# Optimization experiments

Measured on AMD Instinct MI355X. Metric: run time of the kernel, lower is better.

The kernel has to match this reference:

```python
import jax, jax.numpy as jnp
import numpy as np

NUM_TYPES = 4
EPS = 1e-5
NEG_SLOPE = 0.01  # nn.LeakyReLU default


def hetero_linear(x, node_type, W, b):
    # x: [N, Cin], W: [T, Cin, Cout], b: [T, Cout]
    # Grouped GEMM via type-masked batched matmul (T is small and fixed).
    onehot = jax.nn.one_hot(node_type, NUM_TYPES, dtype=x.dtype)  # [N, T]
    xt = onehot.T[:, :, None] * x[None, :, :]                      # [T, N, Cin]
    y = jnp.einsum('tni,tio->no', xt, W)                           # [N, Cout]
    return y + b[node_type]


def hetero_batchnorm(x, node_type, gamma, beta):
    # Per-type batch statistics over the nodes of each type (training-mode BN).
    ones = jnp.ones((x.shape[0],), dtype=x.dtype)
    cnt = jax.ops.segment_sum(ones, node_type, num_segments=NUM_TYPES)      # [T]
    cnt = jnp.maximum(cnt, 1.0)
    s = jax.ops.segment_sum(x, node_type, num_segments=NUM_TYPES)           # [T, C]
    ss = jax.ops.segment_sum(x * x, node_type, num_segments=NUM_TYPES)      # [T, C]
    mean = s / cnt[:, None]
    var = ss / cnt[:, None] - mean * mean  # biased variance, as BN uses
    xn = (x - mean[node_type]) * jax.lax.rsqrt(var[node_type] + EPS)
    return xn * gamma[node_type] + beta[node_type]


def setup_inputs() -> dict:
    key = jax.random.key(0)
    ks = jax.random.split(key, 12)
    N, CIN, H, COUT, T = 32768, 256, 512, 256, NUM_TYPES
    x = jax.random.normal(ks[0], (N, CIN), dtype=jnp.float32)
    node_type = jax.random.randint(ks[1], (N,), 0, T, dtype=jnp.int32)
    def lin(k, ci, co):
        k1, k2 = jax.random.split(k)
        scale = 1.0 / np.sqrt(ci)
        W = jax.random.uniform(k1, (T, ci, co), jnp.float32, -scale, scale)
        b = jax.random.uniform(k2, (T, co), jnp.float32, -scale, scale)
        return W, b
    W1, b1 = lin(ks[2], CIN, H)
    W2, b2 = lin(ks[3], H, H)
    W3, b3 = lin(ks[4], H, COUT)
    gamma1 = jnp.ones((T, H), jnp.float32)
    beta1 = jnp.zeros((T, H), jnp.float32)
    gamma2 = jnp.ones((T, H), jnp.float32)
    beta2 = jnp.zeros((T, H), jnp.float32)
    return {"x": x, "node_type": node_type,
            "W1": W1, "b1": b1, "W2": W2, "b2": b2, "W3": W3, "b3": b3,
            "gamma1": gamma1, "beta1": beta1, "gamma2": gamma2, "beta2": beta2}


def reference(x, node_type, W1, b1, W2, b2, W3, b3, gamma1, beta1, gamma2, beta2):
    # Layer 1: HeteroLinear -> HeteroBatchNorm -> LeakyReLU (dropout p=0 -> identity)
    h = hetero_linear(x, node_type, W1, b1)
    h = hetero_batchnorm(h, node_type, gamma1, beta1)
    h = jax.nn.leaky_relu(h, NEG_SLOPE)
    # Layer 2
    h = hetero_linear(h, node_type, W2, b2)
    h = hetero_batchnorm(h, node_type, gamma2, beta2)
    h = jax.nn.leaky_relu(h, NEG_SLOPE)
    # Layer 3: plain_last -> no norm/act
    out = hetero_linear(h, node_type, W3, b3)
    return out
```

## Files before the change

kernel.cpp:

```cpp
#include <hip/hip_runtime.h>
#include <cstdint>
#include <cstddef>

#define N_NODES 32768
#define CIN 256
#define HDIM 512
#define COUT_F 256
#define NTYPE 4
#define ALIGN_SEG 256
#define NPAD (N_NODES + NTYPE * ALIGN_SEG)
#define NROWBLK (NPAD / 256)
#define BN_EPS 1e-5f
#define SLOPE 0.01f

typedef unsigned short u16;
typedef __attribute__((ext_vector_type(8))) short bf16x8;
typedef __attribute__((ext_vector_type(4))) float f32x4;
typedef __attribute__((ext_vector_type(4))) u16 u16x4;

#define GLOBAL_AS __attribute__((address_space(1)))
#define LDS_AS __attribute__((address_space(3)))
#define SBAR() __builtin_amdgcn_s_barrier()
#define SCHED() __builtin_amdgcn_sched_barrier(0)

__device__ __forceinline__ u16 f2bf(float f) {
  union { float f; unsigned u; } v{f};
  unsigned r = (v.u + 0x7FFF + ((v.u >> 16) & 1)) >> 16;
  return (u16)r;
}
__device__ __forceinline__ float bf2f(u16 b) {
  union { unsigned u; float f; } v;
  v.u = ((unsigned)b) << 16;
  return v.f;
}


__global__ void hist_kernel(const int* __restrict__ nt, int* __restrict__ blockHist) {
  __shared__ int h[NTYPE];
  int tid = threadIdx.x;
  if (tid < NTYPE) h[tid] = 0;
  __syncthreads();
  int i = blockIdx.x * 256 + tid;
  atomicAdd(&h[nt[i]], 1);
  __syncthreads();
  if (tid < NTYPE) blockHist[blockIdx.x * NTYPE + tid] = h[tid];
}

__global__ void scan_kernel(const int* __restrict__ blockHist, int* __restrict__ blockBase,
                            int* __restrict__ meta) {
  int tid = threadIdx.x;
  if (tid < NTYPE) {
    int run = 0;
    for (int b = 0; b < 128; ++b) {
      blockBase[b * NTYPE + tid] = run;
      run += blockHist[b * NTYPE + tid];
    }
    meta[tid] = run;
  }
  __syncthreads();
  if (tid == 0) {
    int s = 0;
    for (int t = 0; t < NTYPE; ++t) {
      meta[4 + t] = s;
      s += (meta[t] + ALIGN_SEG - 1) & ~(ALIGN_SEG - 1);
    }
    meta[8] = s;
  }
}

__global__ void rank_scatter_kernel(const int* __restrict__ nt, const int* __restrict__ blockBase,
                                    const int* __restrict__ meta, int* __restrict__ perm) {
  __shared__ int st[256];
  int tid = threadIdx.x;
  int i = blockIdx.x * 256 + tid;
  int t = nt[i];
  st[tid] = t;
  __syncthreads();
  int rank = 0;
  for (int j = 0; j < tid; ++j) rank += (st[j] == t) ? 1 : 0;
  perm[meta[4 + t] + blockBase[blockIdx.x * NTYPE + t] + rank] = i;
}

__global__ __launch_bounds__(256) void gather_kernel(const float* __restrict__ x,
                                                     const int* __restrict__ perm,
                                                     u16* __restrict__ xs) {
  int p = blockIdx.x * 4 + (threadIdx.x >> 6);
  int lane = threadIdx.x & 63;
  int src = perm[p];
  u16x4* dst = (u16x4*)(xs + (size_t)p * CIN);
  if (src < 0) {
    dst[lane] = (u16x4)0;
  } else {
    float4 v = ((const float4*)(x + (size_t)src * CIN))[lane];
    u16x4 o;
    o.x = f2bf(v.x); o.y = f2bf(v.y); o.z = f2bf(v.z); o.w = f2bf(v.w);
    dst[lane] = o;
  }
}

template <int K, int COUT>
__global__ __launch_bounds__(256) void wtrans_kernel(const float* __restrict__ W,
                                                     u16* __restrict__ Wt) {
  const int t = blockIdx.z;
  const int k0 = blockIdx.x * 32, c0 = blockIdx.y * 32;
  const float* __restrict__ Ws = W + (size_t)t * K * COUT;
  u16* __restrict__ Wd = Wt + (size_t)t * COUT * K;
  __shared__ float tile[32][33];
  int tid = threadIdx.x;
#pragma unroll
  for (int p = 0; p < 4; ++p) {
    int idx = p * 256 + tid;
    int r = idx >> 5, c = idx & 31;
    tile[r][c] = Ws[(size_t)(k0 + r) * COUT + c0 + c];
  }
  __syncthreads();
#pragma unroll
  for (int p = 0; p < 4; ++p) {
    int idx = p * 256 + tid;
    int r = idx >> 5, c = idx & 31;
    Wd[(size_t)(c0 + r) * K + k0 + c] = f2bf(tile[c][r]);
  }
}


template <int K, int COUT, int BN, bool SCATTER, bool STATS>
__global__ __launch_bounds__(512, 2) void mfma_gemm_kernel(
    const u16* __restrict__ A, const u16* __restrict__ Wt, const float* __restrict__ bias,
    u16* __restrict__ Yb, float* __restrict__ Yf, float* __restrict__ partS,
    float* __restrict__ partQ, const int* __restrict__ meta, const int* __restrict__ perm) {
  constexpr int JN = BN / 32;
  constexpr int PB = BN / 64;
  constexpr int GX = COUT / BN;
  constexpr int ASZ = 256 * 64;
  constexpr int BSZ = BN * 64;
  const int nwg = (int)(gridDim.x * gridDim.y);
  int l = (int)(blockIdx.y * gridDim.x + blockIdx.x);
  int lid = (l & 7) * (nwg >> 3) + (l >> 3);
  const int bx = lid % GX, by = lid / GX;
  const int col0 = bx * BN, row0 = by * 256;

  const int s1 = meta[5], s2 = meta[6], s3 = meta[7];
  const int t = row0 >= s3 ? 3 : (row0 >= s2 ? 2 : (row0 >= s1 ? 1 : 0));
  const int seg_end = meta[4 + t] + meta[t];
  const u16* __restrict__ Bt = Wt + (size_t)t * COUT * K;

  __shared__ __align__(16) u16 As[2][ASZ];
  __shared__ __align__(16) u16 Bs[2][BSZ];

  const int tid = threadIdx.x;
  const int lane = tid & 63;
  const int lr = lane & 15, ls = lane >> 4;
  const int wid = tid >> 6;
  const int wm = wid >> 1, wn = wid & 1;

  int a_off[4][2], b_off[JN][2];
#pragma unroll
  for (int i = 0; i < 4; ++i) {
    int r = wm * 64 + i * 16 + lr;
#pragma unroll
    for (int kk = 0; kk < 2; ++kk) a_off[i][kk] = r * 64 + ((kk * 4 + ls) ^ (r & 7)) * 8;
  }
#pragma unroll
  for (int j = 0; j < JN; ++j) {
    int r = wn * (BN / 2) + j * 16 + lr;
#pragma unroll
    for (int kk = 0; kk < 2; ++kk) b_off[j][kk] = r * 64 + ((kk * 4 + ls) ^ (r & 7)) * 8;
  }

  int st_row[4], st_col[4];
#pragma unroll
  for (int p = 0; p < 4; ++p) {
    int lch = p * 512 + tid;
    int r = lch >> 3;
    st_row[p] = r;
    st_col[p] = ((lch & 7) ^ (r & 7)) * 8;
  }
  const int ldsW = (tid & 448) * 8;

  const int nsteps = K / 64;

  auto stage = [&](int buf, int k0) {
#pragma unroll
    for (int p = 0; p < 4; ++p) {
      const u16* ga = A + (size_t)(row0 + st_row[p]) * K + k0 + st_col[p];
      __builtin_amdgcn_global_load_lds((const GLOBAL_AS void*)ga,
                                       (LDS_AS void*)(&As[buf][0] + p * 4096 + ldsW), 16, 0, 0);
    }
#pragma unroll
    for (int p = 0; p < PB; ++p) {
      const u16* gb = Bt + (size_t)(col0 + st_row[p]) * K + k0 + st_col[p];
      __builtin_amdgcn_global_load_lds((const GLOBAL_AS void*)gb,
                                       (LDS_AS void*)(&Bs[buf][0] + p * 4096 + ldsW), 16, 0, 0);
    }
  };

  f32x4 acc[4][JN] = {};

  stage(0, 0);
  for (int t8 = 0; t8 < nsteps; ++t8) {
    const int cur = t8 & 1;
    if (t8 + 1 < nsteps) {
      stage(cur ^ 1, (t8 + 1) * 64);
      if (PB == 4) {
        asm volatile("s_waitcnt vmcnt(8)" ::: "memory");
      } else {
        asm volatile("s_waitcnt vmcnt(6)" ::: "memory");
      }
    } else {
      asm volatile("s_waitcnt vmcnt(0)" ::: "memory");
    }
    SBAR();
    SCHED();
#pragma unroll
    for (int kk = 0; kk < 2; ++kk) {
      bf16x8 af[4], bfr[JN];
#pragma unroll
      for (int i = 0; i < 4; ++i) af[i] = *(const bf16x8*)(&As[cur][0] + a_off[i][kk]);
#pragma unroll
      for (int j = 0; j < JN; ++j) bfr[j] = *(const bf16x8*)(&Bs[cur][0] + b_off[j][kk]);
#pragma unroll
      for (int i = 0; i < 4; ++i)
#pragma unroll
        for (int j = 0; j < JN; ++j)
          acc[i][j] = __builtin_amdgcn_mfma_f32_16x16x32_bf16(af[i], bfr[j], acc[i][j], 0, 0, 0);
    }
    SBAR();
    SCHED();
  }

  float bj[JN];
#pragma unroll
  for (int j = 0; j < JN; ++j)
    bj[j] = bias[(size_t)t * COUT + col0 + wn * (BN / 2) + j * 16 + lr];

  if (SCATTER) {
#pragma unroll
    for (int i = 0; i < 4; ++i) {
      int rbase = row0 + wm * 64 + i * 16 + ls * 4;
      int dsts[4];
#pragma unroll
      for (int r = 0; r < 4; ++r) dsts[r] = perm[rbase + r];
#pragma unroll
      for (int j = 0; j < JN; ++j) {
        int gcol = col0 + wn * (BN / 2) + j * 16 + lr;
#pragma unroll
        for (int r = 0; r < 4; ++r) {
          if (dsts[r] >= 0) Yf[(size_t)dsts[r] * COUT + gcol] = acc[i][j][r] + bj[j];
        }
      }
    }
  } else {
    float s[JN] = {}, q[JN] = {};
#pragma unroll
    for (int i = 0; i < 4; ++i) {
      int rbase = row0 + wm * 64 + i * 16 + ls * 4;
#pragma unroll
      for (int j = 0; j < JN; ++j) {
        int gcol = col0 + wn * (BN / 2) + j * 16 + lr;
#pragma unroll
        for (int r = 0; r < 4; ++r) {
          int row = rbase + r;
          float y = acc[i][j][r] + bj[j];
          Yb[(size_t)row * COUT + gcol] = f2bf(y);
          if (STATS && row < seg_end) {
            s[j] += y;
            q[j] += y * y;
          }
        }
      }
    }
    if (STATS) {
      float* sred = (float*)&As[0][0];
      float* qred = (float*)&Bs[0][0];
      int grp = wm * 4 + ls;
      __syncthreads();
#pragma unroll
      for (int j = 0; j < JN; ++j) {
        int colIdx = wn * (BN / 2) + j * 16 + lr;
        sred[grp * BN + colIdx] = s[j];
        qred[grp * BN + colIdx] = q[j];
      }
      __syncthreads();
      if (tid < BN) {
        float S = 0.f, Q = 0.f;
#pragma unroll
        for (int k = 0; k < 16; ++k) {
          S += sred[k * BN + tid];
          Q += qred[k * BN + tid];
        }
        partS[(size_t)by * COUT + col0 + tid] = S;
        partQ[(size_t)by * COUT + col0 + tid] = Q;
      }
    }
  }
}


__global__ __launch_bounds__(256) void bn_finalize_kernel(const float* __restrict__ partS,
                                                          const float* __restrict__ partQ,
                                                          const int* __restrict__ meta,
                                                          float* __restrict__ mean,
                                                          float* __restrict__ rstd) {
  int idx = blockIdx.x * 256 + threadIdx.x;
  int t = idx >> 9;
  int c = idx & (HDIM - 1);
  int start = meta[4 + t];
  int cnt = meta[t];
  int b0 = start >> 8;
  int nb = (cnt + 255) >> 8;
  float S = 0.f, Q = 0.f;
  for (int b = 0; b < nb; ++b) {
    S += partS[(size_t)(b0 + b) * HDIM + c];
    Q += partQ[(size_t)(b0 + b) * HDIM + c];
  }
  float n = (float)(cnt > 1 ? cnt : 1);
  float m = S / n;
  float var = Q / n - m * m;
  mean[idx] = m;
  rstd[idx] = rsqrtf(fmaxf(var, 0.f) + BN_EPS);
}


__global__ __launch_bounds__(256) void bn_apply_kernel(
    const u16* __restrict__ h, const int* __restrict__ meta, const float* __restrict__ mean,
    const float* __restrict__ rstd, const float* __restrict__ gamma,
    const float* __restrict__ beta, u16* __restrict__ aout) {
  int idx = blockIdx.x * 256 + threadIdx.x;
  int row = idx >> 6;
  int g8 = (idx & 63) * 8;
  const int s1 = meta[5], s2 = meta[6], s3 = meta[7];
  const int t = row >= s3 ? 3 : (row >= s2 ? 2 : (row >= s1 ? 1 : 0));
  size_t base = (size_t)row * HDIM + g8;
  uint4 v = *(const uint4*)(h + base);
  unsigned w[4] = {v.x, v.y, v.z, v.w};
  int tb = t * HDIM + g8;
  float mv[8], rv[8], gv[8], bv[8];
  *(float4*)&mv[0] = *(const float4*)(mean + tb);
  *(float4*)&mv[4] = *(const float4*)(mean + tb + 4);
  *(float4*)&rv[0] = *(const float4*)(rstd + tb);
  *(float4*)&rv[4] = *(const float4*)(rstd + tb + 4);
  *(float4*)&gv[0] = *(const float4*)(gamma + tb);
  *(float4*)&gv[4] = *(const float4*)(gamma + tb + 4);
  *(float4*)&bv[0] = *(const float4*)(beta + tb);
  *(float4*)&bv[4] = *(const float4*)(beta + tb + 4);
  unsigned o[4];
#pragma unroll
  for (int p = 0; p < 4; ++p) {
    u16 lo = (u16)(w[p] & 0xFFFF), hi = (u16)(w[p] >> 16);
    int e0 = p * 2, e1 = p * 2 + 1;
    float sc0 = rv[e0] * gv[e0], sc1 = rv[e1] * gv[e1];
    float y0 = bf2f(lo) * sc0 + (bv[e0] - mv[e0] * sc0);
    float y1 = bf2f(hi) * sc1 + (bv[e1] - mv[e1] * sc1);
    y0 = y0 >= 0.f ? y0 : SLOPE * y0;
    y1 = y1 >= 0.f ? y1 : SLOPE * y1;
    o[p] = (unsigned)f2bf(y0) | ((unsigned)f2bf(y1) << 16);
  }
  *(uint4*)(aout + base) = make_uint4(o[0], o[1], o[2], o[3]);
}


extern "C" void kernel_launch(void* const* d_in, const int* in_sizes, int n_in, void* d_out,
                              int out_size, void* d_ws, size_t ws_size, hipStream_t stream) {
  const float* x = (const float*)d_in[0];
  const int* nt = (const int*)d_in[1];
  const float* W1 = (const float*)d_in[2];
  const float* b1 = (const float*)d_in[3];
  const float* W2 = (const float*)d_in[4];
  const float* b2 = (const float*)d_in[5];
  const float* W3 = (const float*)d_in[6];
  const float* b3 = (const float*)d_in[7];
  const float* g1 = (const float*)d_in[8];
  const float* be1 = (const float*)d_in[9];
  const float* g2 = (const float*)d_in[10];
  const float* be2 = (const float*)d_in[11];
  float* out = (float*)d_out;

  char* ws = (char*)d_ws;
  size_t off = 0;
  auto alloc = [&](size_t bytes) {
    void* p = ws + off;
    off = (off + bytes + 255) & ~(size_t)255;
    return p;
  };
  int* meta = (int*)alloc(16 * 4);
  int* blockHist = (int*)alloc(128 * NTYPE * 4);
  int* blockBase = (int*)alloc(128 * NTYPE * 4);
  int* perm = (int*)alloc((size_t)NPAD * 4);
  float* mean = (float*)alloc((size_t)NTYPE * HDIM * 4);
  float* rstd = (float*)alloc((size_t)NTYPE * HDIM * 4);
  float* partS = (float*)alloc((size_t)NROWBLK * HDIM * 4);
  float* partQ = (float*)alloc((size_t)NROWBLK * HDIM * 4);
  u16* Wt1 = (u16*)alloc((size_t)NTYPE * CIN * HDIM * 2);
  u16* Wt2 = (u16*)alloc((size_t)NTYPE * HDIM * HDIM * 2);
  u16* Wt3 = (u16*)alloc((size_t)NTYPE * HDIM * COUT_F * 2);
  u16* xs = (u16*)alloc((size_t)NPAD * CIN * 2);
  u16* abuf = (u16*)alloc((size_t)NPAD * HDIM * 2);
  u16* hb = (u16*)alloc((size_t)NPAD * HDIM * 2);

  hipMemsetAsync(meta, 0, 64, stream);
  hipMemsetAsync(perm, 0xFF, (size_t)NPAD * 4, stream);
  hist_kernel<<<128, 256, 0, stream>>>(nt, blockHist);
  scan_kernel<<<1, 64, 0, stream>>>(blockHist, blockBase, meta);
  rank_scatter_kernel<<<128, 256, 0, stream>>>(nt, blockBase, meta, perm);
  gather_kernel<<<NPAD / 4, 256, 0, stream>>>(x, perm, xs);

  wtrans_kernel<CIN, HDIM><<<dim3(CIN / 32, HDIM / 32, NTYPE), 256, 0, stream>>>(W1, Wt1);
  wtrans_kernel<HDIM, HDIM><<<dim3(HDIM / 32, HDIM / 32, NTYPE), 256, 0, stream>>>(W2, Wt2);
  wtrans_kernel<HDIM, COUT_F><<<dim3(HDIM / 32, COUT_F / 32, NTYPE), 256, 0, stream>>>(W3, Wt3);

  mfma_gemm_kernel<CIN, HDIM, 256, false, true>
      <<<dim3(HDIM / 256, NPAD / 256), 512, 0, stream>>>(xs, Wt1, b1, hb, nullptr, partS, partQ,
                                                         meta, nullptr);
  bn_finalize_kernel<<<(NTYPE * HDIM) / 256, 256, 0, stream>>>(partS, partQ, meta, mean, rstd);
  bn_apply_kernel<<<(NPAD * (HDIM / 8)) / 256, 256, 0, stream>>>(hb, meta, mean, rstd, g1, be1,
                                                                 abuf);
  mfma_gemm_kernel<HDIM, HDIM, 256, false, true>
      <<<dim3(HDIM / 256, NPAD / 256), 512, 0, stream>>>(abuf, Wt2, b2, hb, nullptr, partS, partQ,
                                                         meta, nullptr);
  bn_finalize_kernel<<<(NTYPE * HDIM) / 256, 256, 0, stream>>>(partS, partQ, meta, mean, rstd);
  bn_apply_kernel<<<(NPAD * (HDIM / 8)) / 256, 256, 0, stream>>>(hb, meta, mean, rstd, g2, be2,
                                                                 abuf);
  mfma_gemm_kernel<HDIM, COUT_F, 128, true, false>
      <<<dim3(COUT_F / 128, NPAD / 256), 512, 0, stream>>>(abuf, Wt3, b3, nullptr, out, nullptr,
                                                           nullptr, meta, perm);
}
```

Baseline: 180.9 us.

## Stage GEMM epilogue through LDS for coalesced stores and shrink column tiles

The GEMM epilogue now writes accumulator tiles into a padded LDS buffer, reusing the staging memory, and then emits wide, row-contiguous 16-byte global stores. In the scatter layer this means one permuted row write per thread instead of strided 4-byte scattered stores. The column tile width is halved in all three GEMMs (256→128, 128→64), which doubles the workgroup count for better CU fill, and the vmcnt waits are adjusted to match. The trade-off is that each A tile is re-read from global memory more often, and the epilogue gains extra LDS round-trips and a barrier.

```diff
diff --git a/kernel.cpp b/kernel.cpp
--- a/kernel.cpp
+++ b/kernel.cpp
@@ -133,6 +133,12 @@
   constexpr int GX = COUT / BN;
   constexpr int ASZ = 256 * 64;
   constexpr int BSZ = BN * 64;
+  constexpr size_t LDS_BYTES = (size_t)(2 * ASZ + 2 * BSZ) * 2;
+
+  __shared__ __align__(16) char LDS_ALL[LDS_BYTES];
+  u16* AsP = (u16*)LDS_ALL;
+  u16* BsP = (u16*)LDS_ALL + 2 * ASZ;
+
   const int nwg = (int)(gridDim.x * gridDim.y);
   int l = (int)(blockIdx.y * gridDim.x + blockIdx.x);
   int lid = (l & 7) * (nwg >> 3) + (l >> 3);
@@ -144,9 +150,6 @@
   const int seg_end = meta[4 + t] + meta[t];
   const u16* __restrict__ Bt = Wt + (size_t)t * COUT * K;
 
-  __shared__ __align__(16) u16 As[2][ASZ];
-  __shared__ __align__(16) u16 Bs[2][BSZ];
-
   const int tid = threadIdx.x;
   const int lane = tid & 63;
   const int lr = lane & 15, ls = lane >> 4;
@@ -184,13 +187,15 @@
     for (int p = 0; p < 4; ++p) {
       const u16* ga = A + (size_t)(row0 + st_row[p]) * K + k0 + st_col[p];
       __builtin_amdgcn_global_load_lds((const GLOBAL_AS void*)ga,
-                                       (LDS_AS void*)(&As[buf][0] + p * 4096 + ldsW), 16, 0, 0);
+                                       (LDS_AS void*)(AsP + buf * ASZ + p * 4096 + ldsW), 16, 0,
+                                       0);
     }
 #pragma unroll
     for (int p = 0; p < PB; ++p) {
       const u16* gb = Bt + (size_t)(col0 + st_row[p]) * K + k0 + st_col[p];
       __builtin_amdgcn_global_load_lds((const GLOBAL_AS void*)gb,
-                                       (LDS_AS void*)(&Bs[buf][0] + p * 4096 + ldsW), 16, 0, 0);
+                                       (LDS_AS void*)(BsP + buf * BSZ + p * 4096 + ldsW), 16, 0,
+                                       0);
     }
   };
 
@@ -201,10 +206,10 @@
     const int cur = t8 & 1;
     if (t8 + 1 < nsteps) {
       stage(cur ^ 1, (t8 + 1) * 64);
-      if (PB == 4) {
-        asm volatile("s_waitcnt vmcnt(8)" ::: "memory");
+      if (PB == 2) {
+        asm volatile("s_waitcnt vmcnt(6)" ::: "memory");
       } else {
-        asm volatile("s_waitcnt vmcnt(6)" ::: "memory");
+        asm volatile("s_waitcnt vmcnt(5)" ::: "memory");
       }
     } else {
       asm volatile("s_waitcnt vmcnt(0)" ::: "memory");
@@ -215,9 +220,9 @@
     for (int kk = 0; kk < 2; ++kk) {
       bf16x8 af[4], bfr[JN];
 #pragma unroll
-      for (int i = 0; i < 4; ++i) af[i] = *(const bf16x8*)(&As[cur][0] + a_off[i][kk]);
-#pragma unroll
-      for (int j = 0; j < JN; ++j) bfr[j] = *(const bf16x8*)(&Bs[cur][0] + b_off[j][kk]);
+      for (int i = 0; i < 4; ++i) af[i] = *(const bf16x8*)(AsP + cur * ASZ + a_off[i][kk]);
+#pragma unroll
+      for (int j = 0; j < JN; ++j) bfr[j] = *(const bf16x8*)(BsP + cur * BSZ + b_off[j][kk]);
 #pragma unroll
       for (int i = 0; i < 4; ++i)
 #pragma unroll
@@ -233,64 +238,82 @@
   for (int j = 0; j < JN; ++j)
     bj[j] = bias[(size_t)t * COUT + col0 + wn * (BN / 2) + j * 16 + lr];
 
-  if (SCATTER) {
-#pragma unroll
-    for (int i = 0; i < 4; ++i) {
-      int rbase = row0 + wm * 64 + i * 16 + ls * 4;
-      int dsts[4];
-#pragma unroll
-      for (int r = 0; r < 4; ++r) dsts[r] = perm[rbase + r];
-#pragma unroll
-      for (int j = 0; j < JN; ++j) {
-        int gcol = col0 + wn * (BN / 2) + j * 16 + lr;
-#pragma unroll
-        for (int r = 0; r < 4; ++r) {
-          if (dsts[r] >= 0) Yf[(size_t)dsts[r] * COUT + gcol] = acc[i][j][r] + bj[j];
-        }
-      }
-    }
-  } else {
-    float s[JN] = {}, q[JN] = {};
-#pragma unroll
-    for (int i = 0; i < 4; ++i) {
-      int rbase = row0 + wm * 64 + i * 16 + ls * 4;
-#pragma unroll
-      for (int j = 0; j < JN; ++j) {
-        int gcol = col0 + wn * (BN / 2) + j * 16 + lr;
-#pragma unroll
-        for (int r = 0; r < 4; ++r) {
-          int row = rbase + r;
-          float y = acc[i][j][r] + bj[j];
-          Yb[(size_t)row * COUT + gcol] = f2bf(y);
-          if (STATS && row < seg_end) {
+  constexpr int CSTRIDE16 = BN + 8;
+  constexpr int CSTRIDE32 = BN + 4;
+  u16* C16 = (u16*)LDS_ALL;
+  float* C32 = (float*)LDS_ALL;
+
+  float s[JN] = {}, q[JN] = {};
+#pragma unroll
+  for (int i = 0; i < 4; ++i) {
+    int rl0 = wm * 64 + i * 16 + ls * 4;
+#pragma unroll
+    for (int j = 0; j < JN; ++j) {
+      int cl = wn * (BN / 2) + j * 16 + lr;
+#pragma unroll
+      for (int r = 0; r < 4; ++r) {
+        float y = acc[i][j][r] + bj[j];
+        if (SCATTER) {
+          C32[(rl0 + r) * CSTRIDE32 + cl] = y;
+        } else {
+          C16[(rl0 + r) * CSTRIDE16 + cl] = f2bf(y);
+          if (STATS && (row0 + rl0 + r) < seg_end) {
             s[j] += y;
             q[j] += y * y;
           }
         }
       }
     }
-    if (STATS) {
-      float* sred = (float*)&As[0][0];
-      float* qred = (float*)&Bs[0][0];
-      int grp = wm * 4 + ls;
-      __syncthreads();
-#pragma unroll
-      for (int j = 0; j < JN; ++j) {
-        int colIdx = wn * (BN / 2) + j * 16 + lr;
-        sred[grp * BN + colIdx] = s[j];
-        qred[grp * BN + colIdx] = q[j];
+  }
+  __syncthreads();
+
+  {
+    int row = tid >> 1, sub = tid & 1;
+    if (SCATTER) {
+      int dst = perm[row0 + row];
+      if (dst >= 0) {
+#pragma unroll
+        for (int c = 0; c < 8; ++c) {
+          int colc = sub * (BN / 2) + c * 4;
+          if (colc < BN) {
+            float4 v = *(const float4*)(C32 + row * CSTRIDE32 + colc);
+            *(float4*)(Yf + (size_t)dst * COUT + col0 + colc) = v;
+          }
+        }
       }
-      __syncthreads();
-      if (tid < BN) {
-        float S = 0.f, Q = 0.f;
-#pragma unroll
-        for (int k = 0; k < 16; ++k) {
-          S += sred[k * BN + tid];
-          Q += qred[k * BN + tid];
+    } else {
+#pragma unroll
+      for (int c = 0; c < 8; ++c) {
+        int colc = sub * (BN / 2) + c * 8;
+        if (colc < BN) {
+          uint4 v = *(const uint4*)(C16 + row * CSTRIDE16 + colc);
+          *(uint4*)(Yb + (size_t)(row0 + row) * COUT + col0 + colc) = v;
         }
-        partS[(size_t)by * COUT + col0 + tid] = S;
-        partQ[(size_t)by * COUT + col0 + tid] = Q;
       }
+    }
+  }
+
+  if (STATS && !SCATTER) {
+    __syncthreads();
+    float* sred = (float*)LDS_ALL;
+    float* qred = (float*)LDS_ALL + 16 * BN;
+    int grp = wm * 4 + ls;
+#pragma unroll
+    for (int j = 0; j < JN; ++j) {
+      int colIdx = wn * (BN / 2) + j * 16 + lr;
+      sred[grp * BN + colIdx] = s[j];
+      qred[grp * BN + colIdx] = q[j];
+    }
+    __syncthreads();
+    if (tid < BN) {
+      float S = 0.f, Q = 0.f;
+#pragma unroll
+      for (int k = 0; k < 16; ++k) {
+        S += sred[k * BN + tid];
+        Q += qred[k * BN + tid];
+      }
+      partS[(size_t)by * COUT + col0 + tid] = S;
+      partQ[(size_t)by * COUT + col0 + tid] = Q;
     }
   }
 }
@@ -408,19 +431,19 @@
   wtrans_kernel<HDIM, HDIM><<<dim3(HDIM / 32, HDIM / 32, NTYPE), 256, 0, stream>>>(W2, Wt2);
   wtrans_kernel<HDIM, COUT_F><<<dim3(HDIM / 32, COUT_F / 32, NTYPE), 256, 0, stream>>>(W3, Wt3);
 
-  mfma_gemm_kernel<CIN, HDIM, 256, false, true>
-      <<<dim3(HDIM / 256, NPAD / 256), 512, 0, stream>>>(xs, Wt1, b1, hb, nullptr, partS, partQ,
+  mfma_gemm_kernel<CIN, HDIM, 128, false, true>
+      <<<dim3(HDIM / 128, NPAD / 256), 512, 0, stream>>>(xs, Wt1, b1, hb, nullptr, partS, partQ,
                                                          meta, nullptr);
   bn_finalize_kernel<<<(NTYPE * HDIM) / 256, 256, 0, stream>>>(partS, partQ, meta, mean, rstd);
   bn_apply_kernel<<<(NPAD * (HDIM / 8)) / 256, 256, 0, stream>>>(hb, meta, mean, rstd, g1, be1,
                                                                  abuf);
-  mfma_gemm_kernel<HDIM, HDIM, 256, false, true>
-      <<<dim3(HDIM / 256, NPAD / 256), 512, 0, stream>>>(abuf, Wt2, b2, hb, nullptr, partS, partQ,
+  mfma_gemm_kernel<HDIM, HDIM, 128, false, true>
+      <<<dim3(HDIM / 128, NPAD / 256), 512, 0, stream>>>(abuf, Wt2, b2, hb, nullptr, partS, partQ,
                                                          meta, nullptr);
   bn_finalize_kernel<<<(NTYPE * HDIM) / 256, 256, 0, stream>>>(partS, partQ, meta, mean, rstd);
   bn_apply_kernel<<<(NPAD * (HDIM / 8)) / 256, 256, 0, stream>>>(hb, meta, mean, rstd, g2, be2,
                                                                  abuf);
-  mfma_gemm_kernel<HDIM, COUT_F, 128, true, false>
-      <<<dim3(COUT_F / 128, NPAD / 256), 512, 0, stream>>>(abuf, Wt3, b3, nullptr, out, nullptr,
-                                                           nullptr, meta, perm);
-}
+  mfma_gemm_kernel<HDIM, COUT_F, 64, true, false>
+      <<<dim3(COUT_F / 64, NPAD / 256), 512, 0, stream>>>(abuf, Wt3, b3, nullptr, out, nullptr,
+                                                          nullptr, meta, perm);
+}
```

Measured after the change: 201.2 us. +11.3%, slower.

## Fuse BatchNorm apply and LeakyReLU into next GEMM's A-operand load

Applied to the files above, without the earlier changes.

The standalone bn_apply passes are removed. The finalize kernel now emits a per-type scale/shift pair, which is staged in LDS. The following GEMM normalizes and activates the A fragments in registers right before the MFMAs. This saves a full read and write of the hidden activation twice per forward pass. In exchange, each workgroup and wave redundantly applies the affine and activation to A tiles, adding VALU work in the inner loop. Output tile widths are also halved (256→128, 128→64), with waitcnt values adjusted, which increases the grid size but also the number of A-tile reloads.

```diff
diff --git a/kernel.cpp b/kernel.cpp
--- a/kernel.cpp
+++ b/kernel.cpp
@@ -123,16 +123,18 @@
 }
 
 
-template <int K, int COUT, int BN, bool SCATTER, bool STATS>
+template <int K, int COUT, int BN, bool APPLY, bool SCATTER, bool STATS>
 __global__ __launch_bounds__(512, 2) void mfma_gemm_kernel(
-    const u16* __restrict__ A, const u16* __restrict__ Wt, const float* __restrict__ bias,
-    u16* __restrict__ Yb, float* __restrict__ Yf, float* __restrict__ partS,
-    float* __restrict__ partQ, const int* __restrict__ meta, const int* __restrict__ perm) {
+    const u16* __restrict__ A, const float* __restrict__ scsh, const u16* __restrict__ Wt,
+    const float* __restrict__ bias, u16* __restrict__ Yb, float* __restrict__ Yf,
+    float* __restrict__ partS, float* __restrict__ partQ, const int* __restrict__ meta,
+    const int* __restrict__ perm) {
   constexpr int JN = BN / 32;
   constexpr int PB = BN / 64;
   constexpr int GX = COUT / BN;
   constexpr int ASZ = 256 * 64;
   constexpr int BSZ = BN * 64;
+
   const int nwg = (int)(gridDim.x * gridDim.y);
   int l = (int)(blockIdx.y * gridDim.x + blockIdx.x);
   int lid = (l & 7) * (nwg >> 3) + (l >> 3);
@@ -146,6 +148,7 @@
 
   __shared__ __align__(16) u16 As[2][ASZ];
   __shared__ __align__(16) u16 Bs[2][BSZ];
+  __shared__ __align__(16) float scshL[2 * HDIM];
 
   const int tid = threadIdx.x;
   const int lane = tid & 63;
@@ -153,6 +156,12 @@
   const int wid = tid >> 6;
   const int wm = wid >> 1, wn = wid & 1;
 
+  if (APPLY) {
+    if (tid < K) {
+      ((float2*)scshL)[tid] = ((const float2*)(scsh + (size_t)t * HDIM * 2))[tid];
+    }
+  }
+
   int a_off[4][2], b_off[JN][2];
 #pragma unroll
   for (int i = 0; i < 4; ++i) {
@@ -201,10 +210,10 @@
     const int cur = t8 & 1;
     if (t8 + 1 < nsteps) {
       stage(cur ^ 1, (t8 + 1) * 64);
-      if (PB == 4) {
-        asm volatile("s_waitcnt vmcnt(8)" ::: "memory");
+      if (PB == 2) {
+        asm volatile("s_waitcnt vmcnt(6)" ::: "memory");
       } else {
-        asm volatile("s_waitcnt vmcnt(6)" ::: "memory");
+        asm volatile("s_waitcnt vmcnt(5)" ::: "memory");
       }
     } else {
       asm volatile("s_waitcnt vmcnt(0)" ::: "memory");
@@ -218,6 +227,22 @@
       for (int i = 0; i < 4; ++i) af[i] = *(const bf16x8*)(&As[cur][0] + a_off[i][kk]);
 #pragma unroll
       for (int j = 0; j < JN; ++j) bfr[j] = *(const bf16x8*)(&Bs[cur][0] + b_off[j][kk]);
+      if (APPLY) {
+        int kb = t8 * 64 + kk * 32 + ls * 8;
+        float2 ss[8];
+#pragma unroll
+        for (int e = 0; e < 8; ++e) ss[e] = ((const float2*)scshL)[kb + e];
+#pragma unroll
+        for (int i = 0; i < 4; ++i) {
+#pragma unroll
+          for (int e = 0; e < 8; ++e) {
+            float z = bf2f((u16)af[i][e]);
+            float y = z * ss[e].x + ss[e].y;
+            y = fmaxf(y, SLOPE * y);
+            af[i][e] = (short)f2bf(y);
+          }
+        }
+      }
 #pragma unroll
       for (int i = 0; i < 4; ++i)
 #pragma unroll
@@ -299,8 +324,9 @@
 __global__ __launch_bounds__(256) void bn_finalize_kernel(const float* __restrict__ partS,
                                                           const float* __restrict__ partQ,
                                                           const int* __restrict__ meta,
-                                                          float* __restrict__ mean,
-                                                          float* __restrict__ rstd) {
+                                                          const float* __restrict__ gamma,
+                                                          const float* __restrict__ beta,
+                                                          float* __restrict__ scsh) {
   int idx = blockIdx.x * 256 + threadIdx.x;
   int t = idx >> 9;
   int c = idx & (HDIM - 1);
@@ -316,46 +342,11 @@
   float n = (float)(cnt > 1 ? cnt : 1);
   float m = S / n;
   float var = Q / n - m * m;
-  mean[idx] = m;
-  rstd[idx] = rsqrtf(fmaxf(var, 0.f) + BN_EPS);
-}
-
-
-__global__ __launch_bounds__(256) void bn_apply_kernel(
-    const u16* __restrict__ h, const int* __restrict__ meta, const float* __restrict__ mean,
-    const float* __restrict__ rstd, const float* __restrict__ gamma,
-    const float* __restrict__ beta, u16* __restrict__ aout) {
-  int idx = blockIdx.x * 256 + threadIdx.x;
-  int row = idx >> 6;
-  int g8 = (idx & 63) * 8;
-  const int s1 = meta[5], s2 = meta[6], s3 = meta[7];
-  const int t = row >= s3 ? 3 : (row >= s2 ? 2 : (row >= s1 ? 1 : 0));
-  size_t base = (size_t)row * HDIM + g8;
-  uint4 v = *(const uint4*)(h + base);
-  unsigned w[4] = {v.x, v.y, v.z, v.w};
-  int tb = t * HDIM + g8;
-  float mv[8], rv[8], gv[8], bv[8];
-  *(float4*)&mv[0] = *(const float4*)(mean + tb);
-  *(float4*)&mv[4] = *(const float4*)(mean + tb + 4);
-  *(float4*)&rv[0] = *(const float4*)(rstd + tb);
-  *(float4*)&rv[4] = *(const float4*)(rstd + tb + 4);
-  *(float4*)&gv[0] = *(const float4*)(gamma + tb);
-  *(float4*)&gv[4] = *(const float4*)(gamma + tb + 4);
-  *(float4*)&bv[0] = *(const float4*)(beta + tb);
-  *(float4*)&bv[4] = *(const float4*)(beta + tb + 4);
-  unsigned o[4];
-#pragma unroll
-  for (int p = 0; p < 4; ++p) {
-    u16 lo = (u16)(w[p] & 0xFFFF), hi = (u16)(w[p] >> 16);
-    int e0 = p * 2, e1 = p * 2 + 1;
-    float sc0 = rv[e0] * gv[e0], sc1 = rv[e1] * gv[e1];
-    float y0 = bf2f(lo) * sc0 + (bv[e0] - mv[e0] * sc0);
-    float y1 = bf2f(hi) * sc1 + (bv[e1] - mv[e1] * sc1);
-    y0 = y0 >= 0.f ? y0 : SLOPE * y0;
-    y1 = y1 >= 0.f ? y1 : SLOPE * y1;
-    o[p] = (unsigned)f2bf(y0) | ((unsigned)f2bf(y1) << 16);
-  }
-  *(uint4*)(aout + base) = make_uint4(o[0], o[1], o[2], o[3]);
+  float rs = rsqrtf(fmaxf(var, 0.f) + BN_EPS);
+  float sc = rs * gamma[idx];
+  float sh = beta[idx] - m * sc;
+  scsh[(size_t)idx * 2] = sc;
+  scsh[(size_t)idx * 2 + 1] = sh;
 }
 
 
@@ -386,16 +377,16 @@
   int* blockHist = (int*)alloc(128 * NTYPE * 4);
   int* blockBase = (int*)alloc(128 * NTYPE * 4);
   int* perm = (int*)alloc((size_t)NPAD * 4);
-  float* mean = (float*)alloc((size_t)NTYPE * HDIM * 4);
-  float* rstd = (float*)alloc((size_t)NTYPE * HDIM * 4);
+  float* scsh1 = (float*)alloc((size_t)NTYPE * HDIM * 2 * 4);
+  float* scsh2 = (float*)alloc((size_t)NTYPE * HDIM * 2 * 4);
   float* partS = (float*)alloc((size_t)NROWBLK * HDIM * 4);
   float* partQ = (float*)alloc((size_t)NROWBLK * HDIM * 4);
   u16* Wt1 = (u16*)alloc((size_t)NTYPE * CIN * HDIM * 2);
   u16* Wt2 = (u16*)alloc((size_t)NTYPE * HDIM * HDIM * 2);
   u16* Wt3 = (u16*)alloc((size_t)NTYPE * HDIM * COUT_F * 2);
   u16* xs = (u16*)alloc((size_t)NPAD * CIN * 2);
-  u16* abuf = (u16*)alloc((size_t)NPAD * HDIM * 2);
-  u16* hb = (u16*)alloc((size_t)NPAD * HDIM * 2);
+  u16* hb1 = (u16*)alloc((size_t)NPAD * HDIM * 2);
+  u16* hb2 = (u16*)alloc((size_t)NPAD * HDIM * 2);
 
   hipMemsetAsync(meta, 0, 64, stream);
   hipMemsetAsync(perm, 0xFF, (size_t)NPAD * 4, stream);
@@ -408,19 +399,15 @@
   wtrans_kernel<HDIM, HDIM><<<dim3(HDIM / 32, HDIM / 32, NTYPE), 256, 0, stream>>>(W2, Wt2);
   wtrans_kernel<HDIM, COUT_F><<<dim3(HDIM / 32, COUT_F / 32, NTYPE), 256, 0, stream>>>(W3, Wt3);
 
-  mfma_gemm_kernel<CIN, HDIM, 256, false, true>
-      <<<dim3(HDIM / 256, NPAD / 256), 512, 0, stream>>>(xs, Wt1, b1, hb, nullptr, partS, partQ,
-                                                         meta, nullptr);
-  bn_finalize_kernel<<<(NTYPE * HDIM) / 256, 256, 0, stream>>>(partS, partQ, meta, mean, rstd);
-  bn_apply_kernel<<<(NPAD * (HDIM / 8)) / 256, 256, 0, stream>>>(hb, meta, mean, rstd, g1, be1,
-                                                                 abuf);
-  mfma_gemm_kernel<HDIM, HDIM, 256, false, true>
-      <<<dim3(HDIM / 256, NPAD / 256), 512, 0, stream>>>(abuf, Wt2, b2, hb, nullptr, partS, partQ,
-                                                         meta, nullptr);
-  bn_finalize_kernel<<<(NTYPE * HDIM) / 256, 256, 0, stream>>>(partS, partQ, meta, mean, rstd);
-  bn_apply_kernel<<<(NPAD * (HDIM / 8)) / 256, 256, 0, stream>>>(hb, meta, mean, rstd, g2, be2,
-                                                                 abuf);
-  mfma_gemm_kernel<HDIM, COUT_F, 128, true, false>
-      <<<dim3(COUT_F / 128, NPAD / 256), 512, 0, stream>>>(abuf, Wt3, b3, nullptr, out, nullptr,
-                                                           nullptr, meta, perm);
-}
+  mfma_gemm_kernel<CIN, HDIM, 128, false, false, true>
+      <<<dim3(HDIM / 128, NPAD / 256), 512, 0, stream>>>(xs, nullptr, Wt1, b1, hb1, nullptr,
+                                                         partS, partQ, meta, nullptr);
+  bn_finalize_kernel<<<(NTYPE * HDIM) / 256, 256, 0, stream>>>(partS, partQ, meta, g1, be1, scsh1);
+  mfma_gemm_kernel<HDIM, HDIM, 128, true, false, true>
+      <<<dim3(HDIM / 128, NPAD / 256), 512, 0, stream>>>(hb1, scsh1, Wt2, b2, hb2, nullptr,
+                                                         partS, partQ, meta, nullptr);
+  bn_finalize_kernel<<<(NTYPE * HDIM) / 256, 256, 0, stream>>>(partS, partQ, meta, g2, be2, scsh2);
+  mfma_gemm_kernel<HDIM, COUT_F, 64, true, true, false>
+      <<<dim3(COUT_F / 64, NPAD / 256), 512, 0, stream>>>(hb2, scsh2, Wt3, b3, nullptr, out,
+                                                          nullptr, nullptr, meta, perm);
+}
```

Result: slower. 214.1 us (+18.4%).
